# Kernel tuning notes

Hardware: AMD Instinct MI355X
Metric: run time of the kernel (lower is better)

## Reference

```python
import jax, jax.numpy as jnp
import numpy as np

D = 768       # embed_dim
DEPTH = 4     # blocks; MoE at odd indices [1,3]
NH = 12       # num_heads
E = 8         # moe_experts
TOPK = 2      # moe_top_k
HID = 3072    # mlp hidden = 4*D
P = 16        # patch size
IMG = 224
NPATCH = (IMG // P) ** 2   # 196
NCLS = 1000


def setup_inputs() -> dict:
    key = jax.random.key(0)
    ks = iter(jax.random.split(key, 48))
    r = lambda shape: jax.random.normal(next(ks), shape, jnp.float32) * 0.02
    inp = {
        'x': jax.random.normal(next(ks), (8, 3, IMG, IMG), jnp.float32),
        'w_patch': r((3 * P * P, D)), 'b_patch': jnp.zeros((D,), jnp.float32),
        'cls_token': r((1, 1, D)), 'pos_embed': r((1, NPATCH + 1, D)),
        'ln1_g': jnp.ones((DEPTH, D), jnp.float32), 'ln1_b': jnp.zeros((DEPTH, D), jnp.float32),
        'w_qkv': r((DEPTH, D, 3 * D)),
        'w_proj': r((DEPTH, D, D)), 'b_proj': jnp.zeros((DEPTH, D), jnp.float32),
        'ln2_g': jnp.ones((DEPTH, D), jnp.float32), 'ln2_b': jnp.zeros((DEPTH, D), jnp.float32),
        'w_fc1': r((2, D, HID)), 'b_fc1': jnp.zeros((2, HID), jnp.float32),
        'w_fc2': r((2, HID, D)), 'b_fc2': jnp.zeros((2, D), jnp.float32),
        'w_gate': r((2, D, E)),
        'w_e1': r((2, E, D, HID)), 'b_e1': jnp.zeros((2, E, HID), jnp.float32),
        'w_e2': r((2, E, HID, D)), 'b_e2': jnp.zeros((2, E, D), jnp.float32),
        'ln_f_g': jnp.ones((D,), jnp.float32), 'ln_f_b': jnp.zeros((D,), jnp.float32),
        'w_head': r((D, NCLS)), 'b_head': jnp.zeros((NCLS,), jnp.float32),
    }
    return inp


def layer_norm(x, g, b, eps=1e-5):
    m = jnp.mean(x, axis=-1, keepdims=True)
    v = jnp.mean(jnp.square(x - m), axis=-1, keepdims=True)
    return (x - m) * jax.lax.rsqrt(v + eps) * g + b


def attention(x, w_qkv, w_proj, b_proj):
    B, N, C = x.shape
    hd = C // NH
    qkv = (x @ w_qkv).reshape(B, N, 3, NH, hd).transpose(2, 0, 3, 1, 4)
    q, k, v = qkv[0], qkv[1], qkv[2]                      # [B, NH, N, hd]
    attn = jax.nn.softmax((q @ k.transpose(0, 1, 3, 2)) * (hd ** -0.5), axis=-1)
    out = (attn @ v).transpose(0, 2, 1, 3).reshape(B, N, C)
    return out @ w_proj + b_proj


def moe_mlp(x, wg, W1, b1, W2, b2):
    # NoisyGate in eval mode: clean logits, top-k, softmax over the k selected logits.
    B, N, C = x.shape
    T = B * N
    xf = x.reshape(T, C)
    logits = xf @ wg                                       # [T, E]
    topv, topi = jax.lax.top_k(logits, TOPK)
    gates = jax.nn.softmax(topv, axis=-1)                  # [T, k]
    gfull = jnp.zeros((T, E), xf.dtype).at[jnp.arange(T)[:, None], topi].add(gates)
    def body(acc, p):
        w1, bb1, w2, bb2, g = p                            # per-expert weights, g: [T]
        h = jax.nn.gelu(xf @ w1 + bb1, approximate=False)  # torch nn.GELU is exact erf
        return acc + g[:, None] * (h @ w2 + bb2), None
    out, _ = jax.lax.scan(body, jnp.zeros_like(xf), (W1, b1, W2, b2, gfull.T))
    return out.reshape(B, N, C)


def reference(x, w_patch, b_patch, cls_token, pos_embed, ln1_g, ln1_b, w_qkv, w_proj,
              b_proj, ln2_g, ln2_b, w_fc1, b_fc1, w_fc2, b_fc2, w_gate, w_e1, b_e1,
              w_e2, b_e2, ln_f_g, ln_f_b, w_head, b_head):
    B = x.shape[0]
    g = IMG // P
    # patchify (equivalent to Conv2d(3, D, P, stride=P))
    patches = x.reshape(B, 3, g, P, g, P).transpose(0, 2, 4, 1, 3, 5).reshape(B, NPATCH, 3 * P * P)
    tok = patches @ w_patch + b_patch                      # [B, 196, D]
    cls = jnp.broadcast_to(cls_token, (B, 1, D))
    h = jnp.concatenate([cls, tok], axis=1) + pos_embed    # [B, 197, D]
    for i in range(DEPTH):
        h = h + attention(layer_norm(h, ln1_g[i], ln1_b[i]), w_qkv[i], w_proj[i], b_proj[i])
        y = layer_norm(h, ln2_g[i], ln2_b[i])
        if i % 2 == 1:
            j = i // 2
            h = h + moe_mlp(y, w_gate[j], w_e1[j], b_e1[j], w_e2[j], b_e2[j])
        else:
            j = i // 2
            h = h + jax.nn.gelu(y @ w_fc1[j] + b_fc1[j], approximate=False) @ w_fc2[j] + b_fc2[j]
    h = layer_norm(h, ln_f_g, ln_f_b)
    return h[:, 0] @ w_head + b_head                       # [B, 1000]
```

## Files before the change

### kernel.cpp

```cpp
#include <hip/hip_runtime.h>
#include <math.h>

#define DD 768
#define NHEAD 12
#define HDIM 64
#define NTOK 197
#define BB 8
#define TT (BB*NTOK)
#define NPATCH 196
#define TP (BB*NPATCH)
#define HID 3072
#define NEXP 8
#define NCLS 1000
#define QKVN (3*DD)
#define MAXA 4224
#define NAT 33
#define NCH 7

#define F_BIAS    1
#define F_GELU    2
#define F_RESID   4
#define F_OUTBF   8
#define F_MOE     16
#define F_GATHER  32
#define F_SCATTER 64

typedef __bf16 bf16_t;
typedef __attribute__((ext_vector_type(8))) __bf16 bf16x8;
typedef __attribute__((ext_vector_type(4))) float f32x4;

__device__ __forceinline__ float gelu_f(float x) {
  return 0.5f * x * (1.0f + erff(x * 0.70710678118654752f));
}

__global__ void tcast_k(const float* __restrict__ src, bf16_t* __restrict__ dst,
                        int K, int N) {
  src += (size_t)blockIdx.z * K * N;
  dst += (size_t)blockIdx.z * K * N;
  __shared__ float t[32][33];
  int n0 = blockIdx.x * 32, k0 = blockIdx.y * 32;
  int tx = threadIdx.x, ty = threadIdx.y;
  #pragma unroll
  for (int i = 0; i < 4; i++)
    t[ty + i*8][tx] = src[(size_t)(k0 + ty + i*8) * N + n0 + tx];
  __syncthreads();
  #pragma unroll
  for (int i = 0; i < 4; i++)
    dst[(size_t)(n0 + ty + i*8) * K + k0 + tx] = (bf16_t)t[tx][ty + i*8];
}

__global__ void patchify_k(const float* __restrict__ x, bf16_t* __restrict__ pm) {
  int idx = blockIdx.x * 256 + threadIdx.x;
  if (idx >= TP * DD) return;
  int cidx = idx % DD;
  int row  = idx / DD;
  int b = row / NPATCH, p = row % NPATCH;
  int c = cidx >> 8;
  int rem = cidx & 255;
  int i = rem >> 4, j = rem & 15;
  int gy = p / 14, gx = p % 14;
  pm[idx] = (bf16_t)x[((size_t)(b*3 + c)*224 + gy*16 + i)*224 + gx*16 + j];
}

__global__ void assemble_k(const float* __restrict__ tok, const float* __restrict__ cls,
                           const float* __restrict__ pos, float* __restrict__ h) {
  int idx = blockIdx.x * 256 + threadIdx.x;
  if (idx >= TT * DD) return;
  int c = idx % DD;
  int row = idx / DD;
  int b = row / NTOK, n = row % NTOK;
  float v;
  if (n == 0) v = cls[c] + pos[c];
  else        v = tok[((size_t)(b*NPATCH + n - 1))*DD + c] + pos[(size_t)n*DD + c];
  h[idx] = v;
}

__global__ void ln_k(const float* __restrict__ in, size_t in_stride,
                     const float* __restrict__ g, const float* __restrict__ bta,
                     float* __restrict__ out, bf16_t* __restrict__ out_bf, int nrows) {
  int r = blockIdx.x;
  if (r >= nrows) return;
  const float* xr = in + (size_t)r * in_stride;
  __shared__ float red[256];
  int tid = threadIdx.x;
  float v0 = xr[tid], v1 = xr[tid+256], v2 = xr[tid+512];
  red[tid] = v0 + v1 + v2; __syncthreads();
  for (int st = 128; st > 0; st >>= 1) { if (tid < st) red[tid] += red[tid+st]; __syncthreads(); }
  float mean = red[0] * (1.0f/768.0f); __syncthreads();
  float d0 = v0-mean, d1 = v1-mean, d2 = v2-mean;
  red[tid] = d0*d0 + d1*d1 + d2*d2; __syncthreads();
  for (int st = 128; st > 0; st >>= 1) { if (tid < st) red[tid] += red[tid+st]; __syncthreads(); }
  float rstd = rsqrtf(red[0] * (1.0f/768.0f) + 1e-5f);
  float o0 = d0*rstd*g[tid]     + bta[tid];
  float o1 = d1*rstd*g[tid+256] + bta[tid+256];
  float o2 = d2*rstd*g[tid+512] + bta[tid+512];
  float* o = out + (size_t)r * DD;
  o[tid] = o0; o[tid+256] = o1; o[tid+512] = o2;
  if (out_bf) {
    bf16_t* ob = out_bf + (size_t)r * DD;
    ob[tid] = (bf16_t)o0; ob[tid+256] = (bf16_t)o1; ob[tid+512] = (bf16_t)o2;
  }
}

__global__ __launch_bounds__(256) void mgemm_k(
    const bf16_t* __restrict__ A, const bf16_t* __restrict__ Bt,
    const float* __restrict__ bias, const float* __restrict__ resid,
    float* __restrict__ Cf, bf16_t* __restrict__ Cb,
    int M, int N, int K, int flags,
    const int* __restrict__ offs, const int* __restrict__ cnt,
    const int* __restrict__ tok_l, const int* __restrict__ slot_l,
    const float* __restrict__ gate_l, float* __restrict__ scat_out) {
  int row0 = blockIdx.y << 7;
  int col0 = blockIdx.x << 7;
  int vend = M;
  const bf16_t* bt = Bt;
  const float* bs = bias;
  if (flags & F_MOE) {
    int total = offs[NEXP];
    if (row0 >= total) return;
    int e = 0;
    #pragma unroll
    for (int q = 1; q < NEXP; q++) if (row0 >= offs[q]) e = q;
    vend = offs[e] + cnt[e];
    bt = Bt + (size_t)e * N * K;
    bs = bias ? bias + (size_t)e * N : bias;
  }
  int tid = threadIdx.x, wave = tid >> 6, lane = tid & 63;
  int r16 = lane & 15, kq = lane >> 4;
  int kq8 = kq << 3;
  __shared__ bf16_t As[128*32];
  __shared__ bf16_t Bs[128*32];
  const bf16_t* aptr[2];
  const bf16_t* bptr[2];
  #pragma unroll
  for (int s = 0; s < 2; s++) {
    int blk = wave*2 + s;
    int rl = (blk << 4) + r16;
    int gr = row0 + rl;
    if (flags & F_GATHER) {
      int t = (gr < vend) ? tok_l[gr] : 0;
      aptr[s] = A + (size_t)t * K;
    } else {
      int cr = gr; if (cr > vend - 1) cr = vend - 1;
      aptr[s] = A + (size_t)cr * K;
    }
    bptr[s] = bt + (size_t)(col0 + rl) * K;
  }
  int woff = (wave*2) * 512 + lane * 8;
  int mi0 = (wave >> 1) * 4, ni0 = (wave & 1) * 4;
  f32x4 acc[4][4];
  #pragma unroll
  for (int i = 0; i < 4; i++)
    #pragma unroll
    for (int j = 0; j < 4; j++)
      acc[i][j] = (f32x4){0.f, 0.f, 0.f, 0.f};

  for (int k0 = 0; k0 < K; k0 += 32) {
    uint4 a0 = *(const uint4*)(aptr[0] + k0 + kq8);
    uint4 a1 = *(const uint4*)(aptr[1] + k0 + kq8);
    uint4 b0 = *(const uint4*)(bptr[0] + k0 + kq8);
    uint4 b1 = *(const uint4*)(bptr[1] + k0 + kq8);
    __syncthreads();
    *(uint4*)&As[woff]       = a0;
    *(uint4*)&As[woff + 512] = a1;
    *(uint4*)&Bs[woff]       = b0;
    *(uint4*)&Bs[woff + 512] = b1;
    __syncthreads();
    bf16x8 af[4], bfr[4];
    #pragma unroll
    for (int i = 0; i < 4; i++) af[i]  = *(const bf16x8*)&As[(mi0+i)*512 + lane*8];
    #pragma unroll
    for (int j = 0; j < 4; j++) bfr[j] = *(const bf16x8*)&Bs[(ni0+j)*512 + lane*8];
    #pragma unroll
    for (int i = 0; i < 4; i++)
      #pragma unroll
      for (int j = 0; j < 4; j++)
        acc[i][j] = __builtin_amdgcn_mfma_f32_16x16x32_bf16(af[i], bfr[j], acc[i][j], 0, 0, 0);
  }

  int rq = kq << 2;
  #pragma unroll
  for (int i = 0; i < 4; i++) {
    #pragma unroll
    for (int p = 0; p < 4; p++) {
      int rr = row0 + ((mi0 + i) << 4) + rq + p;
      if (rr >= vend) continue;
      int t = 0, sl = 0; float gv = 0.f;
      if (flags & F_SCATTER) { t = tok_l[rr]; sl = slot_l[rr]; gv = gate_l[rr]; }
      #pragma unroll
      for (int j = 0; j < 4; j++) {
        int cc = col0 + ((ni0 + j) << 4) + r16;
        float v = acc[i][j][p];
        if (flags & F_BIAS) v += bs[cc];
        if (flags & F_GELU) v = gelu_f(v);
        if (flags & F_SCATTER) {
          scat_out[((size_t)t*2 + sl)*N + cc] = gv * v;
        } else if (flags & F_RESID) {
          Cf[(size_t)rr*N + cc] = v + resid[(size_t)rr*N + cc];
        } else if (flags & F_OUTBF) {
          Cb[(size_t)rr*N + cc] = (bf16_t)v;
        } else {
          Cf[(size_t)rr*N + cc] = v;
        }
      }
    }
  }
}

__global__ __launch_bounds__(256) void fattn_k(const bf16_t* __restrict__ qkv,
                                               bf16_t* __restrict__ out) {
  int qt = blockIdx.x;
  int bh = blockIdx.y;
  int b = bh / NHEAD, hh = bh % NHEAD;
  const bf16_t* base = qkv + (size_t)b * NTOK * QKVN;
  int tid = threadIdx.x, wave = tid >> 6, lane = tid & 63;
  int r16 = lane & 15, kq = lane >> 4;

  __shared__ bf16_t Vt[64 * 232];
  __shared__ bf16_t Ps[4][16 * 40];

  for (int it = 0; it < 56; it++) {
    int idx = it * 256 + tid;
    int d = idx & 63, n = idx >> 6;
    bf16_t bv = (bf16_t)0.f;
    if (n < NTOK) bv = base[(size_t)n * QKVN + 2*DD + hh*HDIM + d];
    Vt[d * 232 + n] = bv;
  }
  __syncthreads();

  int q0 = qt * 64;
  int qrow = q0 + wave * 16 + r16;
  int qr = (qrow < NTOK) ? qrow : 0;
  bf16x8 qf[2];
  #pragma unroll
  for (int ks = 0; ks < 2; ks++)
    qf[ks] = *(const bf16x8*)(base + (size_t)qr * QKVN + hh*HDIM + ks*32 + kq*8);

  f32x4 Oa[4];
  #pragma unroll
  for (int j = 0; j < 4; j++) Oa[j] = (f32x4){0.f,0.f,0.f,0.f};
  float mI[4], lI[4];
  #pragma unroll
  for (int p = 0; p < 4; p++) { mI[p] = -1e30f; lI[p] = 0.f; }

  const bf16_t* Kbase = base + DD + hh*HDIM;
  const bf16x8 zz = {};

  for (int c = 0; c < NCH; c++) {
    f32x4 sc[2];
    sc[0] = (f32x4){0.f,0.f,0.f,0.f};
    sc[1] = (f32x4){0.f,0.f,0.f,0.f};
    #pragma unroll
    for (int tt = 0; tt < 2; tt++) {
      int n = c*32 + tt*16 + r16;
      bool nv = (n < NTOK);
      #pragma unroll
      for (int ks = 0; ks < 2; ks++) {
        bf16x8 kf = zz;
        if (nv) kf = *(const bf16x8*)(Kbase + (size_t)n * QKVN + ks*32 + kq*8);
        sc[tt] = __builtin_amdgcn_mfma_f32_16x16x32_bf16(qf[ks], kf, sc[tt], 0, 0, 0);
      }
    }
    float cm[4];
    #pragma unroll
    for (int p = 0; p < 4; p++) {
      #pragma unroll
      for (int tt = 0; tt < 2; tt++) {
        int col = c*32 + tt*16 + r16;
        float s = sc[tt][p] * 0.125f;
        sc[tt][p] = (col < NTOK) ? s : -1e30f;
      }
      cm[p] = fmaxf(sc[0][p], sc[1][p]);
    }
    #pragma unroll
    for (int off = 1; off < 16; off <<= 1)
      #pragma unroll
      for (int p = 0; p < 4; p++)
        cm[p] = fmaxf(cm[p], __shfl_xor(cm[p], off, 64));
    float al[4], cs[4];
    #pragma unroll
    for (int p = 0; p < 4; p++) {
      float mn = fmaxf(mI[p], cm[p]);
      al[p] = __expf(mI[p] - mn);
      mI[p] = mn;
      float e0 = __expf(sc[0][p] - mn);
      float e1 = __expf(sc[1][p] - mn);
      sc[0][p] = e0; sc[1][p] = e1;
      cs[p] = e0 + e1;
    }
    #pragma unroll
    for (int off = 1; off < 16; off <<= 1)
      #pragma unroll
      for (int p = 0; p < 4; p++)
        cs[p] += __shfl_xor(cs[p], off, 64);
    #pragma unroll
    for (int p = 0; p < 4; p++) lI[p] = lI[p]*al[p] + cs[p];
    #pragma unroll
    for (int j = 0; j < 4; j++)
      #pragma unroll
      for (int p = 0; p < 4; p++)
        Oa[j][p] *= al[p];
    bf16_t* pw = &Ps[wave][0];
    #pragma unroll
    for (int tt = 0; tt < 2; tt++)
      #pragma unroll
      for (int p = 0; p < 4; p++)
        pw[(kq*4+p)*40 + tt*16 + r16] = (bf16_t)sc[tt][p];
    bf16x8 pf = *(const bf16x8*)(pw + r16*40 + kq*8);
    #pragma unroll
    for (int j = 0; j < 4; j++) {
      bf16x8 vf = *(const bf16x8*)(&Vt[(j*16 + r16)*232 + c*32 + kq*8]);
      Oa[j] = __builtin_amdgcn_mfma_f32_16x16x32_bf16(pf, vf, Oa[j], 0, 0, 0);
    }
  }

  #pragma unroll
  for (int p = 0; p < 4; p++) {
    int row = q0 + wave*16 + kq*4 + p;
    if (row >= NTOK) continue;
    float inv = 1.0f / lI[p];
    #pragma unroll
    for (int j = 0; j < 4; j++)
      out[((size_t)b*NTOK + row)*DD + hh*HDIM + j*16 + r16] = (bf16_t)(Oa[j][p] * inv);
  }
}

__global__ void zero_k(int* __restrict__ cnt) {
  if (threadIdx.x < 16) cnt[threadIdx.x] = 0;
}

__global__ void gate_k(const float* __restrict__ xln, const float* __restrict__ wg,
                       int* __restrict__ e01, float* __restrict__ g01, int* __restrict__ cnt) {
  int t = blockIdx.x * 64 + threadIdx.x;
  if (t >= TT) return;
  float lg[NEXP] = {};
  const float* xr = xln + (size_t)t * DD;
  for (int k = 0; k < DD; k++) {
    float xv = xr[k];
    const float* wr = wg + (size_t)k * NEXP;
    #pragma unroll
    for (int e = 0; e < NEXP; e++) lg[e] += xv * wr[e];
  }
  int e0 = 0; float v0 = lg[0];
  #pragma unroll
  for (int e = 1; e < NEXP; e++) if (lg[e] > v0) { v0 = lg[e]; e0 = e; }
  int e1 = -1; float v1 = -1e30f;
  #pragma unroll
  for (int e = 0; e < NEXP; e++) if (e != e0 && lg[e] > v1) { v1 = lg[e]; e1 = e; }
  float g0 = 1.0f / (1.0f + expf(v1 - v0));
  float g1 = 1.0f - g0;
  e01[t*2]   = e0; e01[t*2+1] = e1;
  g01[t*2]   = g0; g01[t*2+1] = g1;
  atomicAdd(&cnt[e0], 1);
  atomicAdd(&cnt[e1], 1);
}

__global__ void offs_k(const int* __restrict__ cnt, int* __restrict__ offs) {
  if (threadIdx.x == 0 && blockIdx.x == 0) {
    int acc = 0;
    for (int e = 0; e < NEXP; e++) {
      offs[e] = acc;
      acc += ((cnt[e] + 127) >> 7) << 7;
    }
    offs[NEXP] = acc;
  }
}

__global__ void scatter_k(const int* __restrict__ e01, const float* __restrict__ g01,
                          const int* __restrict__ offs, int* __restrict__ cnt2,
                          int* __restrict__ tok_l, float* __restrict__ gate_l,
                          int* __restrict__ slot_l) {
  int t = blockIdx.x * 64 + threadIdx.x;
  if (t >= TT) return;
  #pragma unroll
  for (int s = 0; s < 2; s++) {
    int e = e01[t*2+s];
    int pos = atomicAdd(&cnt2[e], 1);
    int a = offs[e] + pos;
    tok_l[a] = t;
    gate_l[a] = g01[t*2+s];
    slot_l[a] = s;
  }
}

__global__ void combine_k(const float* __restrict__ moe_out, float* __restrict__ h) {
  int idx = blockIdx.x * 256 + threadIdx.x;
  if (idx >= TT * DD) return;
  int c = idx % DD;
  int row = idx / DD;
  h[idx] += moe_out[((size_t)row*2)*DD + c] + moe_out[((size_t)row*2 + 1)*DD + c];
}

__global__ void head_k(const float* __restrict__ clsln, const float* __restrict__ w_head,
                       const float* __restrict__ b_head, float* __restrict__ out) {
  int id = blockIdx.x * 256 + threadIdx.x;
  if (id >= BB * NCLS) return;
  int b = id / NCLS, c = id % NCLS;
  float acc = b_head[c];
  const float* xr = clsln + (size_t)b * DD;
  for (int k = 0; k < DD; k++) acc += xr[k] * w_head[(size_t)k*NCLS + c];
  out[id] = acc;
}

extern "C" void kernel_launch(void* const* d_in, const int* in_sizes, int n_in,
                              void* d_out, int out_size, void* d_ws, size_t ws_size,
                              hipStream_t stream) {
  const float* x        = (const float*)d_in[0];
  const float* w_patch  = (const float*)d_in[1];
  const float* b_patch  = (const float*)d_in[2];
  const float* cls_tok  = (const float*)d_in[3];
  const float* pos_emb  = (const float*)d_in[4];
  const float* ln1_g    = (const float*)d_in[5];
  const float* ln1_b    = (const float*)d_in[6];
  const float* w_qkv    = (const float*)d_in[7];
  const float* w_proj   = (const float*)d_in[8];
  const float* b_proj   = (const float*)d_in[9];
  const float* ln2_g    = (const float*)d_in[10];
  const float* ln2_b    = (const float*)d_in[11];
  const float* w_fc1    = (const float*)d_in[12];
  const float* b_fc1    = (const float*)d_in[13];
  const float* w_fc2    = (const float*)d_in[14];
  const float* b_fc2    = (const float*)d_in[15];
  const float* w_gate   = (const float*)d_in[16];
  const float* w_e1     = (const float*)d_in[17];
  const float* b_e1     = (const float*)d_in[18];
  const float* w_e2     = (const float*)d_in[19];
  const float* b_e2     = (const float*)d_in[20];
  const float* ln_f_g   = (const float*)d_in[21];
  const float* ln_f_b   = (const float*)d_in[22];
  const float* w_head   = (const float*)d_in[23];
  const float* b_head   = (const float*)d_in[24];
  float* out = (float*)d_out;
  (void)in_sizes; (void)n_in; (void)out_size; (void)ws_size;

  float* fp = (float*)d_ws;
  float* h      = fp;                          fp += (size_t)TT*DD;
  float* xln    = fp;                          fp += (size_t)TT*DD;
  float* moeout = fp;                          fp += (size_t)TT*2*DD;
  float* clsln  = fp;                          fp += (size_t)8*DD;
  float* g01    = fp;                          fp += (size_t)TT*2;
  float* gate_l = fp;                          fp += (size_t)MAXA;
  int* ip = (int*)fp;
  int* e01    = ip;                            ip += TT*2;
  int* cnt    = ip;                            ip += 8;
  int* cnt2   = ip;                            ip += 8;
  int* offs   = ip;                            ip += 16;
  int* tok_l  = ip;                            ip += MAXA;
  int* slot_l = ip;                            ip += MAXA;
  bf16_t* bp = (bf16_t*)ip;
  bf16_t* pm_bf   = bp;                        bp += (size_t)TP*DD;
  bf16_t* xln_bf  = bp;                        bp += (size_t)TT*DD;
  bf16_t* qkv_bf  = bp;                        bp += (size_t)TT*QKVN;
  bf16_t* attnb   = bp;                        bp += (size_t)TT*DD;
  bf16_t* hid     = bp;                        bp += (size_t)MAXA*HID;
  bf16_t* wT_patch= bp;                        bp += (size_t)DD*DD;
  bf16_t* wT_qkv  = bp;                        bp += (size_t)DD*QKVN;
  bf16_t* wT_proj = bp;                        bp += (size_t)DD*DD;
  bf16_t* wT_big  = bp;                        bp += (size_t)NEXP*DD*HID;

  tcast_k<<<dim3(DD/32, DD/32, 1), dim3(32,8), 0, stream>>>(w_patch, wT_patch, DD, DD);
  patchify_k<<<(TP*DD + 255)/256, 256, 0, stream>>>(x, pm_bf);
  mgemm_k<<<dim3(DD/128, (TP+127)/128), 256, 0, stream>>>(
      pm_bf, wT_patch, b_patch, nullptr, xln, nullptr, TP, DD, DD, F_BIAS,
      nullptr, nullptr, nullptr, nullptr, nullptr, nullptr);
  assemble_k<<<(TT*DD + 255)/256, 256, 0, stream>>>(xln, cls_tok, pos_emb, h);

  const int MT = (TT + 127) / 128;
  for (int i = 0; i < 4; i++) {
    int j = i >> 1;
    tcast_k<<<dim3(QKVN/32, DD/32, 1), dim3(32,8), 0, stream>>>(
        w_qkv + (size_t)i*DD*QKVN, wT_qkv, DD, QKVN);
    tcast_k<<<dim3(DD/32, DD/32, 1), dim3(32,8), 0, stream>>>(
        w_proj + (size_t)i*DD*DD, wT_proj, DD, DD);
    ln_k<<<TT, 256, 0, stream>>>(h, DD, ln1_g + (size_t)i*DD, ln1_b + (size_t)i*DD,
                                 xln, xln_bf, TT);
    mgemm_k<<<dim3(QKVN/128, MT), 256, 0, stream>>>(
        xln_bf, wT_qkv, nullptr, nullptr, nullptr, qkv_bf, TT, QKVN, DD, F_OUTBF,
        nullptr, nullptr, nullptr, nullptr, nullptr, nullptr);
    fattn_k<<<dim3(4, BB*NHEAD), 256, 0, stream>>>(qkv_bf, attnb);
    mgemm_k<<<dim3(DD/128, MT), 256, 0, stream>>>(
        attnb, wT_proj, b_proj + (size_t)i*DD, h, h, nullptr, TT, DD, DD,
        F_BIAS | F_RESID, nullptr, nullptr, nullptr, nullptr, nullptr, nullptr);
    ln_k<<<TT, 256, 0, stream>>>(h, DD, ln2_g + (size_t)i*DD, ln2_b + (size_t)i*DD,
                                 xln, xln_bf, TT);
    if ((i & 1) == 0) {
      tcast_k<<<dim3(HID/32, DD/32, 1), dim3(32,8), 0, stream>>>(
          w_fc1 + (size_t)j*DD*HID, wT_big, DD, HID);
      mgemm_k<<<dim3(HID/128, MT), 256, 0, stream>>>(
          xln_bf, wT_big, b_fc1 + (size_t)j*HID, nullptr, nullptr, hid,
          TT, HID, DD, F_BIAS | F_GELU | F_OUTBF,
          nullptr, nullptr, nullptr, nullptr, nullptr, nullptr);
      tcast_k<<<dim3(DD/32, HID/32, 1), dim3(32,8), 0, stream>>>(
          w_fc2 + (size_t)j*HID*DD, wT_big, HID, DD);
      mgemm_k<<<dim3(DD/128, MT), 256, 0, stream>>>(
          hid, wT_big, b_fc2 + (size_t)j*DD, h, h, nullptr, TT, DD, HID,
          F_BIAS | F_RESID, nullptr, nullptr, nullptr, nullptr, nullptr, nullptr);
    } else {
      zero_k<<<1, 64, 0, stream>>>(cnt);
      gate_k<<<(TT+63)/64, 64, 0, stream>>>(xln, w_gate + (size_t)j*DD*NEXP, e01, g01, cnt);
      offs_k<<<1, 32, 0, stream>>>(cnt, offs);
      scatter_k<<<(TT+63)/64, 64, 0, stream>>>(e01, g01, offs, cnt2, tok_l, gate_l, slot_l);
      tcast_k<<<dim3(HID/32, DD/32, NEXP), dim3(32,8), 0, stream>>>(
          w_e1 + (size_t)j*NEXP*DD*HID, wT_big, DD, HID);
      mgemm_k<<<dim3(HID/128, NAT), 256, 0, stream>>>(
          xln_bf, wT_big, b_e1 + (size_t)j*NEXP*HID, nullptr, nullptr, hid,
          0, HID, DD, F_MOE | F_GATHER | F_BIAS | F_GELU | F_OUTBF,
          offs, cnt, tok_l, nullptr, nullptr, nullptr);
      tcast_k<<<dim3(DD/32, HID/32, NEXP), dim3(32,8), 0, stream>>>(
          w_e2 + (size_t)j*NEXP*HID*DD, wT_big, HID, DD);
      mgemm_k<<<dim3(DD/128, NAT), 256, 0, stream>>>(
          hid, wT_big, b_e2 + (size_t)j*NEXP*DD, nullptr, nullptr, nullptr,
          0, DD, HID, F_MOE | F_SCATTER | F_BIAS,
          offs, cnt, tok_l, slot_l, gate_l, moeout);
      combine_k<<<(TT*DD + 255)/256, 256, 0, stream>>>(moeout, h);
    }
  }

  ln_k<<<8, 256, 0, stream>>>(h, (size_t)NTOK*DD, ln_f_g, ln_f_b, clsln, nullptr, 8);
  head_k<<<(BB*NCLS + 255)/256, 256, 0, stream>>>(clsln, w_head, b_head, out);
}
```

Measured before the change: 1.869 ms.

## Add register prefetch with K=64 steps and 128x64 tiles for narrow GEMMs

Turns the bf16 MFMA GEMM into a template on the N-tile width. The next K=64 slab is prefetched into registers while the current one is consumed from two shared-memory buffers, halving the number of barrier pairs per K. The N=768 GEMMs (patch embed, proj, fc2, expert-2) switch to 128x64 tiles so they launch twice as many blocks on the many compute units. The costs are more registers per thread and smaller per-block reuse for the narrow tiles.

```diff
diff --git a/kernel.cpp b/kernel.cpp
--- a/kernel.cpp
+++ b/kernel.cpp
@@ -102,7 +102,8 @@
   }
 }
 
-__global__ __launch_bounds__(256) void mgemm_k(
+template<int BN>
+__global__ __launch_bounds__(256) void mgemm_t(
     const bf16_t* __restrict__ A, const bf16_t* __restrict__ Bt,
     const float* __restrict__ bias, const float* __restrict__ resid,
     float* __restrict__ Cf, bf16_t* __restrict__ Cb,
@@ -110,8 +111,11 @@
     const int* __restrict__ offs, const int* __restrict__ cnt,
     const int* __restrict__ tok_l, const int* __restrict__ slot_l,
     const float* __restrict__ gate_l, float* __restrict__ scat_out) {
+  constexpr int NB = (BN == 128) ? 2 : 1;
+  constexpr int MI = (BN == 128) ? 4 : 2;
+  constexpr int NJ = 4;
   int row0 = blockIdx.y << 7;
-  int col0 = blockIdx.x << 7;
+  int col0 = blockIdx.x * BN;
   int vend = M;
   const bf16_t* bt = Bt;
   const float* bs = bias;
@@ -128,14 +132,13 @@
   int tid = threadIdx.x, wave = tid >> 6, lane = tid & 63;
   int r16 = lane & 15, kq = lane >> 4;
   int kq8 = kq << 3;
-  __shared__ bf16_t As[128*32];
-  __shared__ bf16_t Bs[128*32];
+  __shared__ bf16_t As[2][128*32];
+  __shared__ bf16_t Bs[2][BN*32];
   const bf16_t* aptr[2];
-  const bf16_t* bptr[2];
+  const bf16_t* bptr[NB];
   #pragma unroll
   for (int s = 0; s < 2; s++) {
-    int blk = wave*2 + s;
-    int rl = (blk << 4) + r16;
+    int rl = ((wave*2 + s) << 4) + r16;
     int gr = row0 + rl;
     if (flags & F_GATHER) {
       int t = (gr < vend) ? tok_l[gr] : 0;
@@ -144,43 +147,75 @@
       int cr = gr; if (cr > vend - 1) cr = vend - 1;
       aptr[s] = A + (size_t)cr * K;
     }
+  }
+  #pragma unroll
+  for (int s = 0; s < NB; s++) {
+    int rl = ((wave*NB + s) << 4) + r16;
     bptr[s] = bt + (size_t)(col0 + rl) * K;
   }
-  int woff = (wave*2) * 512 + lane * 8;
-  int mi0 = (wave >> 1) * 4, ni0 = (wave & 1) * 4;
-  f32x4 acc[4][4];
-  #pragma unroll
-  for (int i = 0; i < 4; i++)
-    #pragma unroll
-    for (int j = 0; j < 4; j++)
+  int woffA = wave*1024 + lane*8;
+  int woffB = wave*NB*512 + lane*8;
+  int mi0 = (BN == 128) ? ((wave >> 1) * 4) : (wave * 2);
+  int ni0 = (BN == 128) ? ((wave & 1) * 4) : 0;
+
+  f32x4 acc[MI][NJ];
+  #pragma unroll
+  for (int i = 0; i < MI; i++)
+    #pragma unroll
+    for (int j = 0; j < NJ; j++)
       acc[i][j] = (f32x4){0.f, 0.f, 0.f, 0.f};
 
-  for (int k0 = 0; k0 < K; k0 += 32) {
-    uint4 a0 = *(const uint4*)(aptr[0] + k0 + kq8);
-    uint4 a1 = *(const uint4*)(aptr[1] + k0 + kq8);
-    uint4 b0 = *(const uint4*)(bptr[0] + k0 + kq8);
-    uint4 b1 = *(const uint4*)(bptr[1] + k0 + kq8);
+  uint4 pa[2][2], pb[NB][2];
+  #pragma unroll
+  for (int s = 0; s < 2; s++)
+    #pragma unroll
+    for (int hh2 = 0; hh2 < 2; hh2++)
+      pa[s][hh2] = *(const uint4*)(aptr[s] + hh2*32 + kq8);
+  #pragma unroll
+  for (int s = 0; s < NB; s++)
+    #pragma unroll
+    for (int hh2 = 0; hh2 < 2; hh2++)
+      pb[s][hh2] = *(const uint4*)(bptr[s] + hh2*32 + kq8);
+
+  for (int k0 = 0; k0 < K; k0 += 64) {
     __syncthreads();
-    *(uint4*)&As[woff]       = a0;
-    *(uint4*)&As[woff + 512] = a1;
-    *(uint4*)&Bs[woff]       = b0;
-    *(uint4*)&Bs[woff + 512] = b1;
+    #pragma unroll
+    for (int hh2 = 0; hh2 < 2; hh2++) {
+      *(uint4*)&As[hh2][woffA]       = pa[0][hh2];
+      *(uint4*)&As[hh2][woffA + 512] = pa[1][hh2];
+      *(uint4*)&Bs[hh2][woffB]       = pb[0][hh2];
+      if (NB == 2) *(uint4*)&Bs[hh2][woffB + 512] = pb[1][hh2];
+    }
     __syncthreads();
-    bf16x8 af[4], bfr[4];
-    #pragma unroll
-    for (int i = 0; i < 4; i++) af[i]  = *(const bf16x8*)&As[(mi0+i)*512 + lane*8];
-    #pragma unroll
-    for (int j = 0; j < 4; j++) bfr[j] = *(const bf16x8*)&Bs[(ni0+j)*512 + lane*8];
-    #pragma unroll
-    for (int i = 0; i < 4; i++)
-      #pragma unroll
-      for (int j = 0; j < 4; j++)
-        acc[i][j] = __builtin_amdgcn_mfma_f32_16x16x32_bf16(af[i], bfr[j], acc[i][j], 0, 0, 0);
+    int kn = (k0 + 64 < K) ? (k0 + 64) : 0;
+    #pragma unroll
+    for (int s = 0; s < 2; s++)
+      #pragma unroll
+      for (int hh2 = 0; hh2 < 2; hh2++)
+        pa[s][hh2] = *(const uint4*)(aptr[s] + kn + hh2*32 + kq8);
+    #pragma unroll
+    for (int s = 0; s < NB; s++)
+      #pragma unroll
+      for (int hh2 = 0; hh2 < 2; hh2++)
+        pb[s][hh2] = *(const uint4*)(bptr[s] + kn + hh2*32 + kq8);
+    #pragma unroll
+    for (int hh2 = 0; hh2 < 2; hh2++) {
+      bf16x8 af[MI], bfr[NJ];
+      #pragma unroll
+      for (int i = 0; i < MI; i++) af[i]  = *(const bf16x8*)&As[hh2][(mi0+i)*512 + lane*8];
+      #pragma unroll
+      for (int j = 0; j < NJ; j++) bfr[j] = *(const bf16x8*)&Bs[hh2][(ni0+j)*512 + lane*8];
+      #pragma unroll
+      for (int i = 0; i < MI; i++)
+        #pragma unroll
+        for (int j = 0; j < NJ; j++)
+          acc[i][j] = __builtin_amdgcn_mfma_f32_16x16x32_bf16(af[i], bfr[j], acc[i][j], 0, 0, 0);
+    }
   }
 
   int rq = kq << 2;
   #pragma unroll
-  for (int i = 0; i < 4; i++) {
+  for (int i = 0; i < MI; i++) {
     #pragma unroll
     for (int p = 0; p < 4; p++) {
       int rr = row0 + ((mi0 + i) << 4) + rq + p;
@@ -188,7 +223,7 @@
       int t = 0, sl = 0; float gv = 0.f;
       if (flags & F_SCATTER) { t = tok_l[rr]; sl = slot_l[rr]; gv = gate_l[rr]; }
       #pragma unroll
-      for (int j = 0; j < 4; j++) {
+      for (int j = 0; j < NJ; j++) {
         int cc = col0 + ((ni0 + j) << 4) + r16;
         float v = acc[i][j][p];
         if (flags & F_BIAS) v += bs[cc];
@@ -460,7 +495,7 @@
 
   tcast_k<<<dim3(DD/32, DD/32, 1), dim3(32,8), 0, stream>>>(w_patch, wT_patch, DD, DD);
   patchify_k<<<(TP*DD + 255)/256, 256, 0, stream>>>(x, pm_bf);
-  mgemm_k<<<dim3(DD/128, (TP+127)/128), 256, 0, stream>>>(
+  mgemm_t<64><<<dim3(DD/64, (TP+127)/128), 256, 0, stream>>>(
       pm_bf, wT_patch, b_patch, nullptr, xln, nullptr, TP, DD, DD, F_BIAS,
       nullptr, nullptr, nullptr, nullptr, nullptr, nullptr);
   assemble_k<<<(TT*DD + 255)/256, 256, 0, stream>>>(xln, cls_tok, pos_emb, h);
@@ -474,11 +509,11 @@
         w_proj + (size_t)i*DD*DD, wT_proj, DD, DD);
     ln_k<<<TT, 256, 0, stream>>>(h, DD, ln1_g + (size_t)i*DD, ln1_b + (size_t)i*DD,
                                  xln, xln_bf, TT);
-    mgemm_k<<<dim3(QKVN/128, MT), 256, 0, stream>>>(
+    mgemm_t<128><<<dim3(QKVN/128, MT), 256, 0, stream>>>(
         xln_bf, wT_qkv, nullptr, nullptr, nullptr, qkv_bf, TT, QKVN, DD, F_OUTBF,
         nullptr, nullptr, nullptr, nullptr, nullptr, nullptr);
     fattn_k<<<dim3(4, BB*NHEAD), 256, 0, stream>>>(qkv_bf, attnb);
-    mgemm_k<<<dim3(DD/128, MT), 256, 0, stream>>>(
+    mgemm_t<64><<<dim3(DD/64, MT), 256, 0, stream>>>(
         attnb, wT_proj, b_proj + (size_t)i*DD, h, h, nullptr, TT, DD, DD,
         F_BIAS | F_RESID, nullptr, nullptr, nullptr, nullptr, nullptr, nullptr);
     ln_k<<<TT, 256, 0, stream>>>(h, DD, ln2_g + (size_t)i*DD, ln2_b + (size_t)i*DD,
@@ -486,13 +521,13 @@
     if ((i & 1) == 0) {
       tcast_k<<<dim3(HID/32, DD/32, 1), dim3(32,8), 0, stream>>>(
           w_fc1 + (size_t)j*DD*HID, wT_big, DD, HID);
-      mgemm_k<<<dim3(HID/128, MT), 256, 0, stream>>>(
+      mgemm_t<128><<<dim3(HID/128, MT), 256, 0, stream>>>(
           xln_bf, wT_big, b_fc1 + (size_t)j*HID, nullptr, nullptr, hid,
           TT, HID, DD, F_BIAS | F_GELU | F_OUTBF,
           nullptr, nullptr, nullptr, nullptr, nullptr, nullptr);
       tcast_k<<<dim3(DD/32, HID/32, 1), dim3(32,8), 0, stream>>>(
           w_fc2 + (size_t)j*HID*DD, wT_big, HID, DD);
-      mgemm_k<<<dim3(DD/128, MT), 256, 0, stream>>>(
+      mgemm_t<64><<<dim3(DD/64, MT), 256, 0, stream>>>(
           hid, wT_big, b_fc2 + (size_t)j*DD, h, h, nullptr, TT, DD, HID,
           F_BIAS | F_RESID, nullptr, nullptr, nullptr, nullptr, nullptr, nullptr);
     } else {
@@ -502,13 +537,13 @@
       scatter_k<<<(TT+63)/64, 64, 0, stream>>>(e01, g01, offs, cnt2, tok_l, gate_l, slot_l);
       tcast_k<<<dim3(HID/32, DD/32, NEXP), dim3(32,8), 0, stream>>>(
           w_e1 + (size_t)j*NEXP*DD*HID, wT_big, DD, HID);
-      mgemm_k<<<dim3(HID/128, NAT), 256, 0, stream>>>(
+      mgemm_t<128><<<dim3(HID/128, NAT), 256, 0, stream>>>(
           xln_bf, wT_big, b_e1 + (size_t)j*NEXP*HID, nullptr, nullptr, hid,
           0, HID, DD, F_MOE | F_GATHER | F_BIAS | F_GELU | F_OUTBF,
           offs, cnt, tok_l, nullptr, nullptr, nullptr);
       tcast_k<<<dim3(DD/32, HID/32, NEXP), dim3(32,8), 0, stream>>>(
           w_e2 + (size_t)j*NEXP*HID*DD, wT_big, HID, DD);
-      mgemm_k<<<dim3(DD/128, NAT), 256, 0, stream>>>(
+      mgemm_t<64><<<dim3(DD/64, NAT), 256, 0, stream>>>(
           hid, wT_big, b_e2 + (size_t)j*NEXP*DD, nullptr, nullptr, nullptr,
           0, DD, HID, F_MOE | F_SCATTER | F_BIAS,
           offs, cnt, tok_l, slot_l, gate_l, moeout);
```

Measured after the change: 2.346 ms. +25.5%, slower.
